# Optimization experiments

Hardware: AMD Instinct MI355X
Metric: run time of the kernel (lower is better)

The kernel has to match this reference:

```python
import jax, jax.numpy as jnp
import numpy as np

N = 100000
K = 32
F_IN = 64
DIMS = [64, 64, 64]

def setup_inputs() -> dict:
    key = jax.random.key(0)
    ks = jax.random.split(key, 10)
    x = jax.random.normal(ks[0], (N, F_IN), dtype=jnp.float32)
    neighbour_indices = jax.random.randint(ks[1], (N, K), 0, N, dtype=jnp.int32)
    distancesq = jax.random.uniform(ks[2], (N, K), dtype=jnp.float32)
    # Dense params: layer 0 takes F_IN; layers i>0 take 2*DIMS[i-1]
    in_dims = [F_IN] + [2 * d for d in DIMS[:-1]]
    params = {}
    for i, (din, dout) in enumerate(zip(in_dims, DIMS)):
        params[f"W{i}"] = jax.random.normal(ks[3 + i], (din, dout), dtype=jnp.float32) * (1.0 / np.sqrt(din))
        params[f"b{i}"] = jnp.zeros((dout,), dtype=jnp.float32)
    return {"x": x, "neighbour_indices": neighbour_indices, "distancesq": distancesq, **params}

def _accumulate_knn(distances, features, indices):
    # distances: [N,K] (already scaled by 10), features: [N,F], indices: [N,K]
    w = jnp.exp(-distances)[..., None]              # [N,K,1]
    g = features[indices]                           # [N,K,F] gather
    wg = w * g
    fmean = jnp.mean(wg, axis=1)                    # [N,F]
    fmax = jnp.max(wg, axis=1)                      # [N,F]
    return jnp.concatenate([fmean, fmax], axis=1)   # [N,2F]

def reference(x, neighbour_indices, distancesq, W0, b0, W1, b1, W2, b2):
    Ws = [W0, W1, W2]
    bs = [b0, b1, b2]
    feats = x
    allfeat = []
    for W, b in zip(Ws, bs):
        feats = jax.nn.relu(feats @ W + b)          # [N,D]
        prev = feats
        feats = _accumulate_knn(10.0 * distancesq, feats, neighbour_indices)  # [N,2D]
        feats = feats - jnp.tile(prev, (1, 2))
        allfeat.append(feats)
    return jnp.concatenate(allfeat + [x], axis=-1)  # [N, F_IN + 2*sum(DIMS)]
```

## Files before the change

### kernel.cpp

```cpp
#include <hip/hip_runtime.h>
#include <math.h>

#define N_NODES    100000
#define K_NEIGH    32
#define OUT_STRIDE 448

typedef __attribute__((ext_vector_type(8))) __bf16 bf16x8;
typedef __attribute__((ext_vector_type(4))) float  f32x4;

static __device__ __forceinline__ unsigned short f2bf(float f) {
    unsigned int u = __float_as_uint(f);
    return (unsigned short)((u + 0x7FFFu + ((u >> 16) & 1u)) >> 16);
}
static __device__ __forceinline__ float bf2f(unsigned short h) {
    return __uint_as_float(((unsigned int)h) << 16);
}

__global__ __launch_bounds__(256) void prep_kernel(
    const float* __restrict__ dist, float* __restrict__ wtab,
    const float* __restrict__ W0, const float* __restrict__ W1,
    const float* __restrict__ W2,
    unsigned short* __restrict__ Wt0, unsigned short* __restrict__ Wt1,
    unsigned short* __restrict__ Wt2)
{
    const int i = blockIdx.x * 256 + threadIdx.x;
    if (i < N_NODES * K_NEIGH) wtab[i] = __expf(-10.f * dist[i]);
    if (i < 64 * 64)  Wt0[(i & 63) * 64  + (i >> 6)] = f2bf(W0[i]);
    if (i < 128 * 64) Wt1[(i & 63) * 128 + (i >> 6)] = f2bf(W1[i]);
    if (i < 128 * 64) Wt2[(i & 63) * 128 + (i >> 6)] = f2bf(W2[i]);
}

template <int DIN, bool COPY_X>
__global__ __launch_bounds__(256) void dense_kernel(
    const float* __restrict__ in, int in_stride,
    const unsigned short* __restrict__ Wt,
    const float* __restrict__ b,
    unsigned short* __restrict__ F, float* __restrict__ out)
{
    constexpr int LDK = DIN + 8;
    __shared__ unsigned short aLDS[64 * LDK];
    __shared__ unsigned short bLDS[64 * LDK];

    const int tid  = threadIdx.x;
    const int row0 = blockIdx.x * 64;

    for (int i = tid; i < 64 * (DIN / 4); i += 256) {
        const int r = i / (DIN / 4);
        const int c = (i % (DIN / 4)) * 4;
        const int n = row0 + r;
        float4 v = make_float4(0.f, 0.f, 0.f, 0.f);
        if (n < N_NODES) {
            v = *(const float4*)&in[(size_t)n * in_stride + c];
            if (COPY_X) *(float4*)&out[(size_t)n * OUT_STRIDE + 384 + c] = v;
        }
        const unsigned int u0 = (unsigned int)f2bf(v.x) | ((unsigned int)f2bf(v.y) << 16);
        const unsigned int u1 = (unsigned int)f2bf(v.z) | ((unsigned int)f2bf(v.w) << 16);
        *(uint2*)&aLDS[r * LDK + c] = make_uint2(u0, u1);
    }
    for (int i = tid; i < 64 * (DIN / 8); i += 256) {
        const int nn = i / (DIN / 8);
        const int k0 = (i % (DIN / 8)) * 8;
        *(uint4*)&bLDS[nn * LDK + k0] = *(const uint4*)&Wt[nn * DIN + k0];
    }
    __syncthreads();

    const int lane = tid & 63;
    const int wv   = tid >> 6;
    const int m    = lane & 15;
    const int quad = lane >> 4;

    f32x4 acc[4];
#pragma unroll
    for (int nb = 0; nb < 4; ++nb) acc[nb] = (f32x4){0.f, 0.f, 0.f, 0.f};

#pragma unroll
    for (int ks = 0; ks < DIN / 32; ++ks) {
        const int koff = ks * 32 + quad * 8;
        const bf16x8 afr =
            *reinterpret_cast<const bf16x8*>(&aLDS[(wv * 16 + m) * LDK + koff]);
#pragma unroll
        for (int nb = 0; nb < 4; ++nb) {
            const bf16x8 bfr =
                *reinterpret_cast<const bf16x8*>(&bLDS[(nb * 16 + m) * LDK + koff]);
            acc[nb] = __builtin_amdgcn_mfma_f32_16x16x32_bf16(afr, bfr, acc[nb], 0, 0, 0);
        }
    }

#pragma unroll
    for (int nb = 0; nb < 4; ++nb) {
        const int c    = nb * 16 + m;
        const float bc = b[c];
#pragma unroll
        for (int reg = 0; reg < 4; ++reg) {
            const int n = row0 + wv * 16 + quad * 4 + reg;
            if (n < N_NODES) {
                const float vv = fmaxf(acc[nb][reg] + bc, 0.f);
                F[(size_t)n * 64 + c] = f2bf(vv);
            }
        }
    }
}

__global__ __launch_bounds__(256) void acc_kernel(
    const unsigned short* __restrict__ F,
    const int* __restrict__ idx,
    const float* __restrict__ wtab,
    float* __restrict__ out)
{
    const int wv   = __builtin_amdgcn_readfirstlane(threadIdx.x >> 6);
    const int lane = threadIdx.x & 63;
    const int n    = blockIdx.x * 4 + wv;

    const float prev = bf2f(F[(size_t)n * 64 + lane]);
    float sum = 0.f;
    float mx  = -INFINITY;

#pragma unroll
    for (int k = 0; k < K_NEIGH; ++k) {
        const int   jk = idx [(size_t)n * K_NEIGH + k];
        const float wk = wtab[(size_t)n * K_NEIGH + k];
        const float g  = bf2f(F[(size_t)jk * 64 + lane]);
        const float v  = wk * g;
        sum += v;
        mx = fmaxf(mx, v);
    }

    out[(size_t)n * OUT_STRIDE + lane]      = sum * (1.f / 32.f) - prev;
    out[(size_t)n * OUT_STRIDE + 64 + lane] = mx - prev;
}

extern "C" void kernel_launch(void* const* d_in, const int* in_sizes, int n_in,
                              void* d_out, int out_size, void* d_ws, size_t ws_size,
                              hipStream_t stream)
{
    const float* x    = (const float*)d_in[0];
    const int*   idx  = (const int*)  d_in[1];
    const float* dist = (const float*)d_in[2];
    const float* W0   = (const float*)d_in[3];
    const float* b0   = (const float*)d_in[4];
    const float* W1   = (const float*)d_in[5];
    const float* b1   = (const float*)d_in[6];
    const float* W2   = (const float*)d_in[7];
    const float* b2   = (const float*)d_in[8];

    float* out = (float*)d_out;

    char* ws = (char*)d_ws;
    unsigned short* F    = (unsigned short*)(ws);
    float*          wtab = (float*)         (ws + 12800000);
    unsigned short* Wt0  = (unsigned short*)(ws + 25600000);
    unsigned short* Wt1  = (unsigned short*)(ws + 25608192);
    unsigned short* Wt2  = (unsigned short*)(ws + 25624576);

    const int prep_grid  = (N_NODES * K_NEIGH + 255) / 256;
    const int dense_grid = (N_NODES + 63) / 64;
    const int acc_grid   = N_NODES / 4;

    prep_kernel<<<prep_grid, 256, 0, stream>>>(dist, wtab, W0, W1, W2, Wt0, Wt1, Wt2);

    dense_kernel<64, true><<<dense_grid, 256, 0, stream>>>(x, 64, Wt0, b0, F, out);
    acc_kernel<<<acc_grid, 256, 0, stream>>>(F, idx, wtab, out + 0);

    dense_kernel<128, false><<<dense_grid, 256, 0, stream>>>(out + 0, OUT_STRIDE, Wt1, b1, F, nullptr);
    acc_kernel<<<acc_grid, 256, 0, stream>>>(F, idx, wtab, out + 128);

    dense_kernel<128, false><<<dense_grid, 256, 0, stream>>>(out + 128, OUT_STRIDE, Wt2, b2, F, nullptr);
    acc_kernel<<<acc_grid, 256, 0, stream>>>(F, idx, wtab, out + 256);
}
```

Measured before the change: 416.9 us.

## Vectorize neighbour gathers with 8 lanes per node and packed index-weight table

```diff
diff --git a/kernel.cpp b/kernel.cpp
--- a/kernel.cpp
+++ b/kernel.cpp
@@ -17,14 +17,16 @@
 }
 
 __global__ __launch_bounds__(256) void prep_kernel(
-    const float* __restrict__ dist, float* __restrict__ wtab,
+    const float* __restrict__ dist, const int* __restrict__ idx,
+    int2* __restrict__ iw,
     const float* __restrict__ W0, const float* __restrict__ W1,
     const float* __restrict__ W2,
     unsigned short* __restrict__ Wt0, unsigned short* __restrict__ Wt1,
     unsigned short* __restrict__ Wt2)
 {
     const int i = blockIdx.x * 256 + threadIdx.x;
-    if (i < N_NODES * K_NEIGH) wtab[i] = __expf(-10.f * dist[i]);
+    if (i < N_NODES * K_NEIGH)
+        iw[i] = make_int2(idx[i], __float_as_int(__expf(-10.f * dist[i])));
     if (i < 64 * 64)  Wt0[(i & 63) * 64  + (i >> 6)] = f2bf(W0[i]);
     if (i < 128 * 64) Wt1[(i & 63) * 128 + (i >> 6)] = f2bf(W1[i]);
     if (i < 128 * 64) Wt2[(i & 63) * 128 + (i >> 6)] = f2bf(W2[i]);
@@ -103,30 +105,63 @@
 
 __global__ __launch_bounds__(256) void acc_kernel(
     const unsigned short* __restrict__ F,
-    const int* __restrict__ idx,
-    const float* __restrict__ wtab,
+    const int2* __restrict__ iw,
     float* __restrict__ out)
 {
-    const int wv   = __builtin_amdgcn_readfirstlane(threadIdx.x >> 6);
-    const int lane = threadIdx.x & 63;
-    const int n    = blockIdx.x * 4 + wv;
-
-    const float prev = bf2f(F[(size_t)n * 64 + lane]);
-    float sum = 0.f;
-    float mx  = -INFINITY;
-
-#pragma unroll
+    const int tid  = threadIdx.x;
+    const int lane = tid & 63;
+    const int wv   = tid >> 6;
+    const int g    = lane >> 3;
+    const int cp   = lane & 7;
+    const int n    = blockIdx.x * 32 + wv * 8 + g;
+
+    const uint4 pv = *(const uint4*)&F[(size_t)n * 64 + cp * 8];
+
+    float sum[8], mx[8];
+#pragma unroll
+    for (int j = 0; j < 8; ++j) { sum[j] = 0.f; mx[j] = -INFINITY; }
+
+    const int2* __restrict__ iwrow = iw + (size_t)n * K_NEIGH;
+
+#pragma unroll 8
     for (int k = 0; k < K_NEIGH; ++k) {
-        const int   jk = idx [(size_t)n * K_NEIGH + k];
-        const float wk = wtab[(size_t)n * K_NEIGH + k];
-        const float g  = bf2f(F[(size_t)jk * 64 + lane]);
-        const float v  = wk * g;
-        sum += v;
-        mx = fmaxf(mx, v);
-    }
-
-    out[(size_t)n * OUT_STRIDE + lane]      = sum * (1.f / 32.f) - prev;
-    out[(size_t)n * OUT_STRIDE + 64 + lane] = mx - prev;
+        const int2  p  = iwrow[k];
+        const float wk = __int_as_float(p.y);
+        const uint4 gv = *(const uint4*)&F[(size_t)p.x * 64 + cp * 8];
+#pragma unroll
+        for (int d = 0; d < 4; ++d) {
+            const unsigned int u = (&gv.x)[d];
+            const float glo = __uint_as_float(u << 16);
+            const float ghi = __uint_as_float(u & 0xffff0000u);
+            const float t0 = wk * glo;
+            const float t1 = wk * ghi;
+            sum[2 * d]     += t0;
+            sum[2 * d + 1] += t1;
+            mx[2 * d]      = fmaxf(mx[2 * d], t0);
+            mx[2 * d + 1]  = fmaxf(mx[2 * d + 1], t1);
+        }
+    }
+
+    float pvf[8];
+#pragma unroll
+    for (int d = 0; d < 4; ++d) {
+        const unsigned int u = (&pv.x)[d];
+        pvf[2 * d]     = __uint_as_float(u << 16);
+        pvf[2 * d + 1] = __uint_as_float(u & 0xffff0000u);
+    }
+
+    float* orow = out + (size_t)n * OUT_STRIDE + cp * 8;
+    const float s = 1.f / 32.f;
+    f32x4 m0 = {sum[0] * s - pvf[0], sum[1] * s - pvf[1],
+                sum[2] * s - pvf[2], sum[3] * s - pvf[3]};
+    f32x4 m1 = {sum[4] * s - pvf[4], sum[5] * s - pvf[5],
+                sum[6] * s - pvf[6], sum[7] * s - pvf[7]};
+    f32x4 x0 = {mx[0] - pvf[0], mx[1] - pvf[1], mx[2] - pvf[2], mx[3] - pvf[3]};
+    f32x4 x1 = {mx[4] - pvf[4], mx[5] - pvf[5], mx[6] - pvf[6], mx[7] - pvf[7]};
+    __builtin_nontemporal_store(m0, (f32x4*)(orow + 0));
+    __builtin_nontemporal_store(m1, (f32x4*)(orow + 4));
+    __builtin_nontemporal_store(x0, (f32x4*)(orow + 64));
+    __builtin_nontemporal_store(x1, (f32x4*)(orow + 68));
 }
 
 extern "C" void kernel_launch(void* const* d_in, const int* in_sizes, int n_in,
@@ -146,24 +181,24 @@
     float* out = (float*)d_out;
 
     char* ws = (char*)d_ws;
-    unsigned short* F    = (unsigned short*)(ws);
-    float*          wtab = (float*)         (ws + 12800000);
-    unsigned short* Wt0  = (unsigned short*)(ws + 25600000);
-    unsigned short* Wt1  = (unsigned short*)(ws + 25608192);
-    unsigned short* Wt2  = (unsigned short*)(ws + 25624576);
+    unsigned short* F   = (unsigned short*)(ws);
+    int2*           iw  = (int2*)          (ws + 12800000);
+    unsigned short* Wt0 = (unsigned short*)(ws + 38400000);
+    unsigned short* Wt1 = (unsigned short*)(ws + 38408192);
+    unsigned short* Wt2 = (unsigned short*)(ws + 38424576);
 
     const int prep_grid  = (N_NODES * K_NEIGH + 255) / 256;
     const int dense_grid = (N_NODES + 63) / 64;
-    const int acc_grid   = N_NODES / 4;
-
-    prep_kernel<<<prep_grid, 256, 0, stream>>>(dist, wtab, W0, W1, W2, Wt0, Wt1, Wt2);
+    const int acc_grid   = N_NODES / 32;
+
+    prep_kernel<<<prep_grid, 256, 0, stream>>>(dist, idx, iw, W0, W1, W2, Wt0, Wt1, Wt2);
 
     dense_kernel<64, true><<<dense_grid, 256, 0, stream>>>(x, 64, Wt0, b0, F, out);
-    acc_kernel<<<acc_grid, 256, 0, stream>>>(F, idx, wtab, out + 0);
+    acc_kernel<<<acc_grid, 256, 0, stream>>>(F, iw, out + 0);
 
     dense_kernel<128, false><<<dense_grid, 256, 0, stream>>>(out + 0, OUT_STRIDE, Wt1, b1, F, nullptr);
-    acc_kernel<<<acc_grid, 256, 0, stream>>>(F, idx, wtab, out + 128);
+    acc_kernel<<<acc_grid, 256, 0, stream>>>(F, iw, out + 128);
 
     dense_kernel<128, false><<<dense_grid, 256, 0, stream>>>(out + 128, OUT_STRIDE, Wt2, b2, F, nullptr);
-    acc_kernel<<<acc_grid, 256, 0, stream>>>(F, idx, wtab, out + 256);
-}
+    acc_kernel<<<acc_grid, 256, 0, stream>>>(F, iw, out + 256);
+}
```

After: 447.9 us. 1.07x slower.

## Split features into channel slabs and pack neighbour index with quantized weight

Applied to the files above, without the earlier changes.

```diff
diff --git a/kernel.cpp b/kernel.cpp
--- a/kernel.cpp
+++ b/kernel.cpp
@@ -4,6 +4,7 @@
 #define N_NODES    100000
 #define K_NEIGH    32
 #define OUT_STRIDE 448
+#define SLAB       (N_NODES * 16)
 
 typedef __attribute__((ext_vector_type(8))) __bf16 bf16x8;
 typedef __attribute__((ext_vector_type(4))) float  f32x4;
@@ -17,14 +18,19 @@
 }
 
 __global__ __launch_bounds__(256) void prep_kernel(
-    const float* __restrict__ dist, float* __restrict__ wtab,
+    const float* __restrict__ dist, const int* __restrict__ idx,
+    unsigned int* __restrict__ iwp,
     const float* __restrict__ W0, const float* __restrict__ W1,
     const float* __restrict__ W2,
     unsigned short* __restrict__ Wt0, unsigned short* __restrict__ Wt1,
     unsigned short* __restrict__ Wt2)
 {
     const int i = blockIdx.x * 256 + threadIdx.x;
-    if (i < N_NODES * K_NEIGH) wtab[i] = __expf(-10.f * dist[i]);
+    if (i < N_NODES * K_NEIGH) {
+        const float w = __expf(-10.f * dist[i]);
+        const unsigned int w15 = (unsigned int)(w * 32767.f + 0.5f);
+        iwp[i] = ((unsigned int)idx[i] << 15) | w15;
+    }
     if (i < 64 * 64)  Wt0[(i & 63) * 64  + (i >> 6)] = f2bf(W0[i]);
     if (i < 128 * 64) Wt1[(i & 63) * 128 + (i >> 6)] = f2bf(W1[i]);
     if (i < 128 * 64) Wt2[(i & 63) * 128 + (i >> 6)] = f2bf(W2[i]);
@@ -95,7 +101,7 @@
             const int n = row0 + wv * 16 + quad * 4 + reg;
             if (n < N_NODES) {
                 const float vv = fmaxf(acc[nb][reg] + bc, 0.f);
-                F[(size_t)n * 64 + c] = f2bf(vv);
+                F[(size_t)nb * SLAB + (size_t)n * 16 + m] = f2bf(vv);
             }
         }
     }
@@ -103,30 +109,75 @@
 
 __global__ __launch_bounds__(256) void acc_kernel(
     const unsigned short* __restrict__ F,
-    const int* __restrict__ idx,
-    const float* __restrict__ wtab,
+    const unsigned int* __restrict__ iwp,
     float* __restrict__ out)
 {
-    const int wv   = __builtin_amdgcn_readfirstlane(threadIdx.x >> 6);
-    const int lane = threadIdx.x & 63;
-    const int n    = blockIdx.x * 4 + wv;
-
-    const float prev = bf2f(F[(size_t)n * 64 + lane]);
-    float sum = 0.f;
-    float mx  = -INFINITY;
+    __shared__ unsigned int iwLDS[64 * 36];
+
+    const int pass  = blockIdx.x & 3;
+    const int chunk = blockIdx.x >> 2;
+    const int node0 = chunk * 64;
+    const int tid   = threadIdx.x;
+
+    for (int t = tid; t < 512; t += 256) {
+        const int r  = t >> 3;
+        const int k0 = (t & 7) * 4;
+        uint4 v = make_uint4(0u, 0u, 0u, 0u);
+        if (node0 + r < N_NODES)
+            v = *(const uint4*)&iwp[(size_t)(node0 + r) * K_NEIGH + k0];
+        *(uint4*)&iwLDS[r * 36 + k0] = v;
+    }
+    __syncthreads();
+
+    const int lane = tid & 63;
+    const int wv   = tid >> 6;
+    const int g    = lane >> 2;
+    const int cp   = lane & 3;
+    const int r    = wv * 16 + g;
+    const int n    = node0 + r;
+
+    const unsigned short* __restrict__ Fs = F + (size_t)pass * SLAB;
+
+    float sum[4], mx[4];
+#pragma unroll
+    for (int j = 0; j < 4; ++j) { sum[j] = 0.f; mx[j] = -INFINITY; }
 
 #pragma unroll
     for (int k = 0; k < K_NEIGH; ++k) {
-        const int   jk = idx [(size_t)n * K_NEIGH + k];
-        const float wk = wtab[(size_t)n * K_NEIGH + k];
-        const float g  = bf2f(F[(size_t)jk * 64 + lane]);
-        const float v  = wk * g;
-        sum += v;
-        mx = fmaxf(mx, v);
-    }
-
-    out[(size_t)n * OUT_STRIDE + lane]      = sum * (1.f / 32.f) - prev;
-    out[(size_t)n * OUT_STRIDE + 64 + lane] = mx - prev;
+        const unsigned int u  = iwLDS[r * 36 + k];
+        const float        wk = (float)(u & 0x7FFFu) * (1.f / 32767.f);
+        const unsigned int jk = u >> 15;
+        const uint2 gv = *(const uint2*)&Fs[(size_t)jk * 16 + cp * 4];
+#pragma unroll
+        for (int d = 0; d < 2; ++d) {
+            const unsigned int uu = (&gv.x)[d];
+            const float t0 = wk * __uint_as_float(uu << 16);
+            const float t1 = wk * __uint_as_float(uu & 0xffff0000u);
+            sum[2 * d]     += t0;
+            sum[2 * d + 1] += t1;
+            mx[2 * d]      = fmaxf(mx[2 * d], t0);
+            mx[2 * d + 1]  = fmaxf(mx[2 * d + 1], t1);
+        }
+    }
+
+    if (n < N_NODES) {
+        const uint2 pv = *(const uint2*)&Fs[(size_t)n * 16 + cp * 4];
+        float pvf[4];
+#pragma unroll
+        for (int d = 0; d < 2; ++d) {
+            const unsigned int uu = (&pv.x)[d];
+            pvf[2 * d]     = __uint_as_float(uu << 16);
+            pvf[2 * d + 1] = __uint_as_float(uu & 0xffff0000u);
+        }
+        const float s = 1.f / 32.f;
+        f32x4 vm = {sum[0] * s - pvf[0], sum[1] * s - pvf[1],
+                    sum[2] * s - pvf[2], sum[3] * s - pvf[3]};
+        f32x4 vx = {mx[0] - pvf[0], mx[1] - pvf[1],
+                    mx[2] - pvf[2], mx[3] - pvf[3]};
+        float* orow = out + (size_t)n * OUT_STRIDE + pass * 16 + cp * 4;
+        __builtin_nontemporal_store(vm, (f32x4*)(orow));
+        __builtin_nontemporal_store(vx, (f32x4*)(orow + 64));
+    }
 }
 
 extern "C" void kernel_launch(void* const* d_in, const int* in_sizes, int n_in,
@@ -146,24 +197,24 @@
     float* out = (float*)d_out;
 
     char* ws = (char*)d_ws;
-    unsigned short* F    = (unsigned short*)(ws);
-    float*          wtab = (float*)         (ws + 12800000);
-    unsigned short* Wt0  = (unsigned short*)(ws + 25600000);
-    unsigned short* Wt1  = (unsigned short*)(ws + 25608192);
-    unsigned short* Wt2  = (unsigned short*)(ws + 25624576);
+    unsigned short* F   = (unsigned short*)(ws);
+    unsigned int*   iwp = (unsigned int*)  (ws + 12800000);
+    unsigned short* Wt0 = (unsigned short*)(ws + 25600000);
+    unsigned short* Wt1 = (unsigned short*)(ws + 25608192);
+    unsigned short* Wt2 = (unsigned short*)(ws + 25624576);
 
     const int prep_grid  = (N_NODES * K_NEIGH + 255) / 256;
     const int dense_grid = (N_NODES + 63) / 64;
-    const int acc_grid   = N_NODES / 4;
-
-    prep_kernel<<<prep_grid, 256, 0, stream>>>(dist, wtab, W0, W1, W2, Wt0, Wt1, Wt2);
+    const int acc_grid   = 4 * ((N_NODES + 63) / 64);
+
+    prep_kernel<<<prep_grid, 256, 0, stream>>>(dist, idx, iwp, W0, W1, W2, Wt0, Wt1, Wt2);
 
     dense_kernel<64, true><<<dense_grid, 256, 0, stream>>>(x, 64, Wt0, b0, F, out);
-    acc_kernel<<<acc_grid, 256, 0, stream>>>(F, idx, wtab, out + 0);
+    acc_kernel<<<acc_grid, 256, 0, stream>>>(F, iwp, out + 0);
 
     dense_kernel<128, false><<<dense_grid, 256, 0, stream>>>(out + 0, OUT_STRIDE, Wt1, b1, F, nullptr);
-    acc_kernel<<<acc_grid, 256, 0, stream>>>(F, idx, wtab, out + 128);
+    acc_kernel<<<acc_grid, 256, 0, stream>>>(F, iwp, out + 128);
 
     dense_kernel<128, false><<<dense_grid, 256, 0, stream>>>(out + 128, OUT_STRIDE, Wt2, b2, F, nullptr);
-    acc_kernel<<<acc_grid, 256, 0, stream>>>(F, idx, wtab, out + 256);
-}
+    acc_kernel<<<acc_grid, 256, 0, stream>>>(F, iwp, out + 256);
+}
```

Result: slower. 453.6 us (+8.8%).
